# Optimization experiments

Hardware: AMD Instinct MI355X
Metric: run time of the kernel (lower is better)

The kernel has to match this reference:

```python
import jax, jax.numpy as jnp
import numpy as np

E = 1024
H = 16
DFF = 4 * E
EPS = 1e-5


def layer_norm(x, scale, bias):
    mu = jnp.mean(x, axis=-1, keepdims=True)
    var = jnp.var(x, axis=-1, keepdims=True)
    return (x - mu) * jax.lax.rsqrt(var + EPS) * scale + bias


def setup_inputs() -> dict:
    key = jax.random.key(0)
    ks = jax.random.split(key, 12)
    N, L = 2, 2048
    x = jax.random.normal(ks[0], (N, L, E), dtype=jnp.float32)
    attn_mask = jax.random.randint(ks[1], (N, H, L, L), 0, 2) == 1
    s = 0.02
    return {
        "x": x,
        "attn_mask": attn_mask,
        "ln1_s": jnp.ones((E,), jnp.float32),
        "ln1_b": jnp.zeros((E,), jnp.float32),
        "Wqkv": jax.random.normal(ks[2], (E, 3 * E), jnp.float32) * s,
        "bqkv": jnp.zeros((3 * E,), jnp.float32),
        "Wo": jax.random.normal(ks[3], (E, E), jnp.float32) * s,
        "bo": jnp.zeros((E,), jnp.float32),
        "ln2_s": jnp.ones((E,), jnp.float32),
        "ln2_b": jnp.zeros((E,), jnp.float32),
        "lnf_s": jnp.ones((E,), jnp.float32),
        "lnf_b": jnp.zeros((E,), jnp.float32),
        "W1": jax.random.normal(ks[4], (E, DFF), jnp.float32) * s,
        "b1": jnp.zeros((DFF,), jnp.float32),
        "W2": jax.random.normal(ks[5], (DFF, E), jnp.float32) * s,
        "b2": jnp.zeros((E,), jnp.float32),
    }


def reference(x, attn_mask, ln1_s, ln1_b, Wqkv, bqkv, Wo, bo,
              ln2_s, ln2_b, lnf_s, lnf_b, W1, b1, W2, b2):
    N, L, _ = x.shape
    D = E // H
    # --- self attention (pre-norm) ---
    h = layer_norm(x, ln1_s, ln1_b)
    qkv = h @ Wqkv + bqkv                      # [N,L,3E]
    q, k, v = jnp.split(qkv, 3, axis=-1)
    q = q.reshape(N, L, H, D)
    k = k.reshape(N, L, H, D)
    v = v.reshape(N, L, H, D)
    a = jnp.einsum('nqhd,nkhd->nhqk', q, k) * (D ** -0.5)  # [N,H,L,L]
    a = jnp.where(attn_mask, -jnp.inf, a)
    a = jax.nn.softmax(a, axis=-1)
    o = jnp.einsum('nhqk,nkhd->nqhd', a, v).reshape(N, L, E)
    o = o @ Wo + bo
    x = x + o
    # --- feedforward (norm_2 then FF's internal LN) ---
    h = layer_norm(x, ln2_s, ln2_b)
    h = layer_norm(h, lnf_s, lnf_b)
    h = jax.nn.gelu(h @ W1 + b1, approximate=False) @ W2 + b2
    return x + h
```

## Files before the change

kernel.cpp:

```cpp
#include <hip/hip_runtime.h>
#include <math.h>

#define E_DIM 1024
#define H_HEADS 16
#define D_HEAD 64
#define DFF_DIM 4096
#define L_SEQ 2048
#define N_BATCH 2
#define T_TOK (N_BATCH * L_SEQ)

typedef __attribute__((ext_vector_type(8))) __bf16 bf16x8;
typedef __attribute__((ext_vector_type(4))) float f32x4;

__device__ __forceinline__ unsigned short f2bf(float f) {
  union { float f; unsigned int u; } v; v.f = f;
  unsigned int r = v.u + 0x7fffu + ((v.u >> 16) & 1u);
  return (unsigned short)(r >> 16);
}

__global__ __launch_bounds__(256) void convert_transpose(
    const float* __restrict__ in, unsigned short* __restrict__ out, int K, int N) {
  __shared__ float tile[32][33];
  int n0 = blockIdx.x * 32, k0 = blockIdx.y * 32;
  int tx = threadIdx.x & 31, ty = threadIdx.x >> 5;
#pragma unroll
  for (int i = 0; i < 32; i += 8)
    tile[ty + i][tx] = in[(size_t)(k0 + ty + i) * N + n0 + tx];
  __syncthreads();
#pragma unroll
  for (int i = 0; i < 32; i += 8)
    out[(size_t)(n0 + ty + i) * K + k0 + tx] = f2bf(tile[tx][ty + i]);
}

__device__ __forceinline__ void block_reduce2(float& a, float& b, float* sm, int tid) {
#pragma unroll
  for (int off = 32; off > 0; off >>= 1) {
    a += __shfl_down(a, off);
    b += __shfl_down(b, off);
  }
  int wid = tid >> 6;
  if ((tid & 63) == 0) { sm[wid * 2] = a; sm[wid * 2 + 1] = b; }
  __syncthreads();
  a = sm[0] + sm[2] + sm[4] + sm[6];
  b = sm[1] + sm[3] + sm[5] + sm[7];
}

__global__ __launch_bounds__(256) void ln_kernel(
    const float* __restrict__ x, const float* __restrict__ s,
    const float* __restrict__ b, unsigned short* __restrict__ out) {
  int row = blockIdx.x, tid = threadIdx.x;
  __shared__ float sm[8];
  float4 v = ((const float4*)(x + (size_t)row * E_DIM))[tid];
  float sum = v.x + v.y + v.z + v.w;
  float sq = v.x * v.x + v.y * v.y + v.z * v.z + v.w * v.w;
  block_reduce2(sum, sq, sm, tid);
  float mu = sum * (1.0f / E_DIM);
  float var = sq * (1.0f / E_DIM) - mu * mu;
  float rs = rsqrtf(var + 1e-5f);
  float4 sv = ((const float4*)s)[tid];
  float4 bv = ((const float4*)b)[tid];
  ushort4 o4;
  o4.x = f2bf((v.x - mu) * rs * sv.x + bv.x);
  o4.y = f2bf((v.y - mu) * rs * sv.y + bv.y);
  o4.z = f2bf((v.z - mu) * rs * sv.z + bv.z);
  o4.w = f2bf((v.w - mu) * rs * sv.w + bv.w);
  ((ushort4*)(out + (size_t)row * E_DIM))[tid] = o4;
}

__global__ __launch_bounds__(256) void ln2_kernel(
    const float* __restrict__ x, const float* __restrict__ s2,
    const float* __restrict__ b2, const float* __restrict__ sf,
    const float* __restrict__ bf_, unsigned short* __restrict__ out) {
  int row = blockIdx.x, tid = threadIdx.x;
  __shared__ float sm[8];
  float4 v = ((const float4*)(x + (size_t)row * E_DIM))[tid];
  float sum = v.x + v.y + v.z + v.w;
  float sq = v.x * v.x + v.y * v.y + v.z * v.z + v.w * v.w;
  block_reduce2(sum, sq, sm, tid);
  float mu = sum * (1.0f / E_DIM);
  float rs = rsqrtf(sq * (1.0f / E_DIM) - mu * mu + 1e-5f);
  float4 s2v = ((const float4*)s2)[tid];
  float4 b2v = ((const float4*)b2)[tid];
  float y0 = (v.x - mu) * rs * s2v.x + b2v.x;
  float y1 = (v.y - mu) * rs * s2v.y + b2v.y;
  float y2 = (v.z - mu) * rs * s2v.z + b2v.z;
  float y3 = (v.w - mu) * rs * s2v.w + b2v.w;
  float sum2 = y0 + y1 + y2 + y3;
  float sq2 = y0 * y0 + y1 * y1 + y2 * y2 + y3 * y3;
  __syncthreads();
  block_reduce2(sum2, sq2, sm, tid);
  float mu2 = sum2 * (1.0f / E_DIM);
  float rs2 = rsqrtf(sq2 * (1.0f / E_DIM) - mu2 * mu2 + 1e-5f);
  float4 sfv = ((const float4*)sf)[tid];
  float4 bfv = ((const float4*)bf_)[tid];
  ushort4 o4;
  o4.x = f2bf((y0 - mu2) * rs2 * sfv.x + bfv.x);
  o4.y = f2bf((y1 - mu2) * rs2 * sfv.y + bfv.y);
  o4.z = f2bf((y2 - mu2) * rs2 * sfv.z + bfv.z);
  o4.w = f2bf((y3 - mu2) * rs2 * sfv.w + bfv.w);
  ((ushort4*)(out + (size_t)row * E_DIM))[tid] = o4;
}

template <int EPI>
__global__ __launch_bounds__(256) void gemm_bt(
    const unsigned short* __restrict__ A, const unsigned short* __restrict__ Bt,
    const float* __restrict__ bias, const float* __restrict__ resid,
    void* __restrict__ outp, int M, int N, int K) {
  __shared__ unsigned short As[128 * 40];
  __shared__ unsigned short Bs[128 * 40];
  int tid = threadIdx.x;
  int lane = tid & 63, wave = tid >> 6;
  int m0 = blockIdx.y * 128, n0 = blockIdx.x * 128;
  int wm = (wave & 1) * 64, wn = (wave >> 1) * 64;
  int lm = lane & 15, lq = lane >> 4;
  int trow = tid >> 2, tcol = tid & 3;
  f32x4 acc[4][4] = {};
  for (int k0 = 0; k0 < K; k0 += 32) {
    uint4 av0 = *(const uint4*)(A + (size_t)(m0 + trow) * K + k0 + tcol * 8);
    uint4 av1 = *(const uint4*)(A + (size_t)(m0 + trow + 64) * K + k0 + tcol * 8);
    uint4 bv0 = *(const uint4*)(Bt + (size_t)(n0 + trow) * K + k0 + tcol * 8);
    uint4 bv1 = *(const uint4*)(Bt + (size_t)(n0 + trow + 64) * K + k0 + tcol * 8);
    __syncthreads();
    *(uint4*)(As + trow * 40 + tcol * 8) = av0;
    *(uint4*)(As + (trow + 64) * 40 + tcol * 8) = av1;
    *(uint4*)(Bs + trow * 40 + tcol * 8) = bv0;
    *(uint4*)(Bs + (trow + 64) * 40 + tcol * 8) = bv1;
    __syncthreads();
    bf16x8 a[4], b[4];
#pragma unroll
    for (int i = 0; i < 4; i++)
      a[i] = *(const bf16x8*)(As + (wm + i * 16 + lm) * 40 + lq * 8);
#pragma unroll
    for (int j = 0; j < 4; j++)
      b[j] = *(const bf16x8*)(Bs + (wn + j * 16 + lm) * 40 + lq * 8);
#pragma unroll
    for (int i = 0; i < 4; i++)
#pragma unroll
      for (int j = 0; j < 4; j++)
        acc[i][j] = __builtin_amdgcn_mfma_f32_16x16x32_bf16(a[i], b[j], acc[i][j], 0, 0, 0);
  }
#pragma unroll
  for (int i = 0; i < 4; i++)
#pragma unroll
    for (int j = 0; j < 4; j++) {
      int row = m0 + wm + i * 16 + lq * 4;
      int col = n0 + wn + j * 16 + lm;
      float bcol = bias[col];
#pragma unroll
      for (int r = 0; r < 4; r++) {
        float v = acc[i][j][r] + bcol;
        size_t idx = (size_t)(row + r) * N + col;
        if (EPI == 0) {
          ((unsigned short*)outp)[idx] = f2bf(v);
        } else if (EPI == 1) {
          float g = 0.5f * v * (1.0f + erff(v * 0.70710678118f));
          ((unsigned short*)outp)[idx] = f2bf(g);
        } else {
          ((float*)outp)[idx] = resid[idx] + v;
        }
      }
    }
}

__global__ __launch_bounds__(256) void attn_kernel(
    const unsigned short* __restrict__ qkv, const int* __restrict__ mask,
    unsigned short* __restrict__ o) {
  const int bq = blockIdx.x;
  const int nh = blockIdx.y;
  const int h = nh & 15;
  const int tid = threadIdx.x, lane = tid & 63, wave = tid >> 6;
  const int lm = lane & 15, lq = lane >> 4;

  __shared__ unsigned short Ks[64 * 72];
  __shared__ unsigned short Vs[64 * 66];
  __shared__ unsigned short Ps[4][16 * 72];

  const int q_base = bq * 64;
  const int tok0 = (nh >> 4) * L_SEQ;
  const int qoff = h * 64, koff = E_DIM + h * 64, voff = 2 * E_DIM + h * 64;
  const int* mbase = mask + (size_t)nh * L_SEQ * L_SEQ;

  bf16x8 qf[2];
  {
    int t = tok0 + q_base + wave * 16 + lm;
    const unsigned short* qr = qkv + (size_t)t * (3 * E_DIM) + qoff + lq * 8;
    qf[0] = *(const bf16x8*)(qr);
    qf[1] = *(const bf16x8*)(qr + 32);
  }

  float m_run[4], l_run[4];
  f32x4 oacc[4] = {};
#pragma unroll
  for (int r = 0; r < 4; r++) { m_run[r] = -1e30f; l_run[r] = 0.0f; }

  for (int kt = 0; kt < L_SEQ / 64; kt++) {
    const int k_base = kt * 64;
    __syncthreads();
    {
      int row = tid >> 3, chunk = tid & 7;
#pragma unroll
      for (int it = 0; it < 2; it++) {
        int key = row + it * 32;
        int t = tok0 + k_base + key;
        uint4 kv = *(const uint4*)(qkv + (size_t)t * (3 * E_DIM) + koff + chunk * 8);
        *(uint4*)(Ks + key * 72 + chunk * 8) = kv;
        uint4 vv = *(const uint4*)(qkv + (size_t)t * (3 * E_DIM) + voff + chunk * 8);
        unsigned int* vw = (unsigned int*)(Vs + key * 66 + chunk * 8);
        vw[0] = vv.x; vw[1] = vv.y; vw[2] = vv.z; vw[3] = vv.w;
      }
    }
    __syncthreads();

    f32x4 s[4];
#pragma unroll
    for (int nt = 0; nt < 4; nt++) {
      bf16x8 kb0 = *(const bf16x8*)(Ks + (nt * 16 + lm) * 72 + lq * 8);
      bf16x8 kb1 = *(const bf16x8*)(Ks + (nt * 16 + lm) * 72 + 32 + lq * 8);
      f32x4 acc = {};
      acc = __builtin_amdgcn_mfma_f32_16x16x32_bf16(qf[0], kb0, acc, 0, 0, 0);
      acc = __builtin_amdgcn_mfma_f32_16x16x32_bf16(qf[1], kb1, acc, 0, 0, 0);
      s[nt] = acc;
    }
    const int qrow = q_base + wave * 16 + lq * 4;
#pragma unroll
    for (int nt = 0; nt < 4; nt++) {
      int kcol = k_base + nt * 16 + lm;
#pragma unroll
      for (int r = 0; r < 4; r++) {
        float v = s[nt][r] * 0.125f;
        int mval = mbase[(size_t)(qrow + r) * L_SEQ + kcol];
        s[nt][r] = mval ? -1e30f : v;
      }
    }
    float alpha[4], rsum[4];
#pragma unroll
    for (int r = 0; r < 4; r++) {
      float v = fmaxf(fmaxf(s[0][r], s[1][r]), fmaxf(s[2][r], s[3][r]));
#pragma unroll
      for (int mo = 1; mo < 16; mo <<= 1) v = fmaxf(v, __shfl_xor(v, mo));
      float mn = fmaxf(m_run[r], v);
      alpha[r] = __expf(m_run[r] - mn);
      m_run[r] = mn;
      rsum[r] = 0.0f;
    }
    unsigned short* pw = Ps[wave];
#pragma unroll
    for (int nt = 0; nt < 4; nt++)
#pragma unroll
      for (int r = 0; r < 4; r++) {
        float p = __expf(s[nt][r] - m_run[r]);
        rsum[r] += p;
        pw[(lq * 4 + r) * 72 + nt * 16 + lm] = f2bf(p);
      }
#pragma unroll
    for (int r = 0; r < 4; r++) {
      float v = rsum[r];
#pragma unroll
      for (int mo = 1; mo < 16; mo <<= 1) v += __shfl_xor(v, mo);
      l_run[r] = l_run[r] * alpha[r] + v;
    }
#pragma unroll
    for (int j = 0; j < 4; j++)
#pragma unroll
      for (int r = 0; r < 4; r++) oacc[j][r] *= alpha[r];
    __syncthreads();

#pragma unroll
    for (int c = 0; c < 2; c++) {
      bf16x8 pa = *(const bf16x8*)(pw + lm * 72 + c * 32 + lq * 8);
#pragma unroll
      for (int j = 0; j < 4; j++) {
        bf16x8 vb;
#pragma unroll
        for (int jj = 0; jj < 8; jj++)
          vb[jj] = *(const __bf16*)(Vs + (c * 32 + lq * 8 + jj) * 66 + j * 16 + lm);
        oacc[j] = __builtin_amdgcn_mfma_f32_16x16x32_bf16(pa, vb, oacc[j], 0, 0, 0);
      }
    }
  }
  const int qrow = q_base + wave * 16 + lq * 4;
#pragma unroll
  for (int r = 0; r < 4; r++) {
    float inv_l = 1.0f / l_run[r];
    int t = tok0 + qrow + r;
#pragma unroll
    for (int j = 0; j < 4; j++)
      o[(size_t)t * E_DIM + h * 64 + j * 16 + lm] = f2bf(oacc[j][r] * inv_l);
  }
}

extern "C" void kernel_launch(void* const* d_in, const int* in_sizes, int n_in,
                              void* d_out, int out_size, void* d_ws, size_t ws_size,
                              hipStream_t stream) {
  const float* x = (const float*)d_in[0];
  const int* mask = (const int*)d_in[1];
  const float* ln1_s = (const float*)d_in[2];
  const float* ln1_b = (const float*)d_in[3];
  const float* Wqkv = (const float*)d_in[4];
  const float* bqkv = (const float*)d_in[5];
  const float* Wo = (const float*)d_in[6];
  const float* bo = (const float*)d_in[7];
  const float* ln2_s = (const float*)d_in[8];
  const float* ln2_b = (const float*)d_in[9];
  const float* lnf_s = (const float*)d_in[10];
  const float* lnf_b = (const float*)d_in[11];
  const float* W1 = (const float*)d_in[12];
  const float* b1 = (const float*)d_in[13];
  const float* W2 = (const float*)d_in[14];
  const float* b2 = (const float*)d_in[15];

  size_t off = 0;
  auto alloc = [&](size_t bytes) {
    void* p = (char*)d_ws + off;
    off += (bytes + 255) & ~(size_t)255;
    return p;
  };
  unsigned short* WqkvT = (unsigned short*)alloc((size_t)3072 * 1024 * 2);
  unsigned short* WoT = (unsigned short*)alloc((size_t)1024 * 1024 * 2);
  unsigned short* W1T = (unsigned short*)alloc((size_t)4096 * 1024 * 2);
  unsigned short* W2T = (unsigned short*)alloc((size_t)1024 * 4096 * 2);
  unsigned short* h1 = (unsigned short*)alloc((size_t)T_TOK * E_DIM * 2);
  unsigned short* qkvb = (unsigned short*)alloc((size_t)T_TOK * 3 * E_DIM * 2);
  unsigned short* ob = (unsigned short*)alloc((size_t)T_TOK * E_DIM * 2);
  float* x2 = (float*)alloc((size_t)T_TOK * E_DIM * 4);
  unsigned short* h2 = (unsigned short*)alloc((size_t)T_TOK * E_DIM * 2);
  unsigned short* g1 = (unsigned short*)alloc((size_t)T_TOK * DFF_DIM * 2);

  convert_transpose<<<dim3(3072 / 32, 1024 / 32), 256, 0, stream>>>(Wqkv, WqkvT, 1024, 3072);
  convert_transpose<<<dim3(1024 / 32, 1024 / 32), 256, 0, stream>>>(Wo, WoT, 1024, 1024);
  convert_transpose<<<dim3(4096 / 32, 1024 / 32), 256, 0, stream>>>(W1, W1T, 1024, 4096);
  convert_transpose<<<dim3(1024 / 32, 4096 / 32), 256, 0, stream>>>(W2, W2T, 4096, 1024);
  ln_kernel<<<T_TOK, 256, 0, stream>>>(x, ln1_s, ln1_b, h1);
  gemm_bt<0><<<dim3(3072 / 128, T_TOK / 128), 256, 0, stream>>>(
      h1, WqkvT, bqkv, nullptr, qkvb, T_TOK, 3072, 1024);
  attn_kernel<<<dim3(L_SEQ / 64, N_BATCH * H_HEADS), 256, 0, stream>>>(qkvb, mask, ob);
  gemm_bt<2><<<dim3(1024 / 128, T_TOK / 128), 256, 0, stream>>>(
      ob, WoT, bo, x, x2, T_TOK, 1024, 1024);
  ln2_kernel<<<T_TOK, 256, 0, stream>>>(x2, ln2_s, ln2_b, lnf_s, lnf_b, h2);
  gemm_bt<1><<<dim3(DFF_DIM / 128, T_TOK / 128), 256, 0, stream>>>(
      h2, W1T, b1, nullptr, g1, T_TOK, DFF_DIM, 1024);
  gemm_bt<2><<<dim3(1024 / 128, T_TOK / 128), 256, 0, stream>>>(
      g1, W2T, b2, x2, (float*)d_out, T_TOK, 1024, 4096);

  (void)in_sizes; (void)n_in; (void)out_size; (void)ws_size;
}
```

Measured before the change: 1.073 ms.

## Use direct global-to-LDS loads, swizzled K tiles, and transposed V in attention

The GEMM tile loads now go straight from global memory into LDS with the global_load_lds builtin, which removes the register staging and the padded LDS rows. In attention, K tiles are also loaded directly into LDS with an XOR swizzle to avoid bank conflicts, and V is stored transposed so each MFMA B operand is one vector LDS read instead of eight scalar reads. Mask loads are issued early, before the tile barrier, so their latency overlaps the LDS fill. The risks are bank conflicts in the unpadded GEMM LDS layout, scattered 2-byte writes for the V transpose, and correctness of the LDS placement that global_load_lds implies.

```diff
diff --git a/kernel.cpp b/kernel.cpp
--- a/kernel.cpp
+++ b/kernel.cpp
@@ -16,6 +16,12 @@
   union { float f; unsigned int u; } v; v.f = f;
   unsigned int r = v.u + 0x7fffu + ((v.u >> 16) & 1u);
   return (unsigned short)(r >> 16);
+}
+
+__device__ __forceinline__ void gl2lds16(const void* g, void* l) {
+  __builtin_amdgcn_global_load_lds(
+      (const __attribute__((address_space(1))) unsigned int*)g,
+      (__attribute__((address_space(3))) unsigned int*)l, 16, 0, 0);
 }
 
 __global__ __launch_bounds__(256) void convert_transpose(
@@ -106,33 +112,37 @@
     const unsigned short* __restrict__ A, const unsigned short* __restrict__ Bt,
     const float* __restrict__ bias, const float* __restrict__ resid,
     void* __restrict__ outp, int M, int N, int K) {
-  __shared__ unsigned short As[128 * 40];
-  __shared__ unsigned short Bs[128 * 40];
+  __shared__ unsigned short As[128 * 32];
+  __shared__ unsigned short Bs[128 * 32];
   int tid = threadIdx.x;
   int lane = tid & 63, wave = tid >> 6;
   int m0 = blockIdx.y * 128, n0 = blockIdx.x * 128;
   int wm = (wave & 1) * 64, wn = (wave >> 1) * 64;
   int lm = lane & 15, lq = lane >> 4;
-  int trow = tid >> 2, tcol = tid & 3;
+
+  int r0 = tid >> 2, coff = (tid & 3) * 8;
+  const unsigned short* Abase = A + (size_t)m0 * K;
+  const unsigned short* Bbase = Bt + (size_t)n0 * K;
+  unsigned short* lA0 = As + (tid >> 6) * 512;
+  unsigned short* lA1 = As + 2048 + (tid >> 6) * 512;
+  unsigned short* lB0 = Bs + (tid >> 6) * 512;
+  unsigned short* lB1 = Bs + 2048 + (tid >> 6) * 512;
+
   f32x4 acc[4][4] = {};
   for (int k0 = 0; k0 < K; k0 += 32) {
-    uint4 av0 = *(const uint4*)(A + (size_t)(m0 + trow) * K + k0 + tcol * 8);
-    uint4 av1 = *(const uint4*)(A + (size_t)(m0 + trow + 64) * K + k0 + tcol * 8);
-    uint4 bv0 = *(const uint4*)(Bt + (size_t)(n0 + trow) * K + k0 + tcol * 8);
-    uint4 bv1 = *(const uint4*)(Bt + (size_t)(n0 + trow + 64) * K + k0 + tcol * 8);
-    __syncthreads();
-    *(uint4*)(As + trow * 40 + tcol * 8) = av0;
-    *(uint4*)(As + (trow + 64) * 40 + tcol * 8) = av1;
-    *(uint4*)(Bs + trow * 40 + tcol * 8) = bv0;
-    *(uint4*)(Bs + (trow + 64) * 40 + tcol * 8) = bv1;
+    __syncthreads();
+    gl2lds16(Abase + (size_t)r0 * K + k0 + coff, lA0);
+    gl2lds16(Abase + (size_t)(r0 + 64) * K + k0 + coff, lA1);
+    gl2lds16(Bbase + (size_t)r0 * K + k0 + coff, lB0);
+    gl2lds16(Bbase + (size_t)(r0 + 64) * K + k0 + coff, lB1);
     __syncthreads();
     bf16x8 a[4], b[4];
 #pragma unroll
     for (int i = 0; i < 4; i++)
-      a[i] = *(const bf16x8*)(As + (wm + i * 16 + lm) * 40 + lq * 8);
+      a[i] = *(const bf16x8*)(As + (wm + i * 16 + lm) * 32 + lq * 8);
 #pragma unroll
     for (int j = 0; j < 4; j++)
-      b[j] = *(const bf16x8*)(Bs + (wn + j * 16 + lm) * 40 + lq * 8);
+      b[j] = *(const bf16x8*)(Bs + (wn + j * 16 + lm) * 32 + lq * 8);
 #pragma unroll
     for (int i = 0; i < 4; i++)
 #pragma unroll
@@ -171,8 +181,8 @@
   const int tid = threadIdx.x, lane = tid & 63, wave = tid >> 6;
   const int lm = lane & 15, lq = lane >> 4;
 
-  __shared__ unsigned short Ks[64 * 72];
-  __shared__ unsigned short Vs[64 * 66];
+  __shared__ unsigned short Ks[64 * 64];
+  __shared__ unsigned short Vt[64 * 72];
   __shared__ unsigned short Ps[4][16 * 72];
 
   const int q_base = bq * 64;
@@ -188,6 +198,12 @@
     qf[1] = *(const bf16x8*)(qr + 32);
   }
 
+  const int sk0 = tid >> 3, sc0 = tid & 7;
+  unsigned short* lK0 = Ks + (tid >> 6) * 512;
+  unsigned short* lK1 = Ks + 2048 + (tid >> 6) * 512;
+  const int vkey = tid >> 3, vchunk = tid & 7;
+  const int qrow = q_base + wave * 16 + lq * 4;
+
   float m_run[4], l_run[4];
   f32x4 oacc[4] = {};
 #pragma unroll
@@ -196,17 +212,26 @@
   for (int kt = 0; kt < L_SEQ / 64; kt++) {
     const int k_base = kt * 64;
     __syncthreads();
+    gl2lds16(qkv + (size_t)(tok0 + k_base + sk0) * (3 * E_DIM) + koff +
+                 ((sc0 ^ (sk0 & 7)) * 8), lK0);
+    gl2lds16(qkv + (size_t)(tok0 + k_base + sk0 + 32) * (3 * E_DIM) + koff +
+                 ((sc0 ^ ((sk0 + 32) & 7)) * 8), lK1);
+    uint4 vv0 = *(const uint4*)(qkv + (size_t)(tok0 + k_base + vkey) * (3 * E_DIM) + voff + vchunk * 8);
+    uint4 vv1 = *(const uint4*)(qkv + (size_t)(tok0 + k_base + vkey + 32) * (3 * E_DIM) + voff + vchunk * 8);
+    int mv[4][4];
+#pragma unroll
+    for (int nt = 0; nt < 4; nt++)
+#pragma unroll
+      for (int r = 0; r < 4; r++)
+        mv[nt][r] = mbase[(size_t)(qrow + r) * L_SEQ + k_base + nt * 16 + lm];
     {
-      int row = tid >> 3, chunk = tid & 7;
-#pragma unroll
-      for (int it = 0; it < 2; it++) {
-        int key = row + it * 32;
-        int t = tok0 + k_base + key;
-        uint4 kv = *(const uint4*)(qkv + (size_t)t * (3 * E_DIM) + koff + chunk * 8);
-        *(uint4*)(Ks + key * 72 + chunk * 8) = kv;
-        uint4 vv = *(const uint4*)(qkv + (size_t)t * (3 * E_DIM) + voff + chunk * 8);
-        unsigned int* vw = (unsigned int*)(Vs + key * 66 + chunk * 8);
-        vw[0] = vv.x; vw[1] = vv.y; vw[2] = vv.z; vw[3] = vv.w;
+      const unsigned short* p0 = (const unsigned short*)&vv0;
+      const unsigned short* p1 = (const unsigned short*)&vv1;
+#pragma unroll
+      for (int jj = 0; jj < 8; jj++) {
+        int jx = (jj + vchunk) & 7;
+        Vt[(vchunk * 8 + jx) * 72 + vkey] = p0[jx];
+        Vt[(vchunk * 8 + jx) * 72 + vkey + 32] = p1[jx];
       }
     }
     __syncthreads();
@@ -214,24 +239,21 @@
     f32x4 s[4];
 #pragma unroll
     for (int nt = 0; nt < 4; nt++) {
-      bf16x8 kb0 = *(const bf16x8*)(Ks + (nt * 16 + lm) * 72 + lq * 8);
-      bf16x8 kb1 = *(const bf16x8*)(Ks + (nt * 16 + lm) * 72 + 32 + lq * 8);
+      int key = nt * 16 + lm, sw = key & 7;
+      bf16x8 kb0 = *(const bf16x8*)(Ks + key * 64 + ((lq ^ sw) * 8));
+      bf16x8 kb1 = *(const bf16x8*)(Ks + key * 64 + (((lq + 4) ^ sw) * 8));
       f32x4 acc = {};
       acc = __builtin_amdgcn_mfma_f32_16x16x32_bf16(qf[0], kb0, acc, 0, 0, 0);
       acc = __builtin_amdgcn_mfma_f32_16x16x32_bf16(qf[1], kb1, acc, 0, 0, 0);
       s[nt] = acc;
     }
-    const int qrow = q_base + wave * 16 + lq * 4;
-#pragma unroll
-    for (int nt = 0; nt < 4; nt++) {
-      int kcol = k_base + nt * 16 + lm;
+#pragma unroll
+    for (int nt = 0; nt < 4; nt++)
 #pragma unroll
       for (int r = 0; r < 4; r++) {
         float v = s[nt][r] * 0.125f;
-        int mval = mbase[(size_t)(qrow + r) * L_SEQ + kcol];
-        s[nt][r] = mval ? -1e30f : v;
-      }
-    }
+        s[nt][r] = mv[nt][r] ? -1e30f : v;
+      }
     float alpha[4], rsum[4];
 #pragma unroll
     for (int r = 0; r < 4; r++) {
@@ -270,15 +292,11 @@
       bf16x8 pa = *(const bf16x8*)(pw + lm * 72 + c * 32 + lq * 8);
 #pragma unroll
       for (int j = 0; j < 4; j++) {
-        bf16x8 vb;
-#pragma unroll
-        for (int jj = 0; jj < 8; jj++)
-          vb[jj] = *(const __bf16*)(Vs + (c * 32 + lq * 8 + jj) * 66 + j * 16 + lm);
+        bf16x8 vb = *(const bf16x8*)(Vt + (j * 16 + lm) * 72 + c * 32 + lq * 8);
         oacc[j] = __builtin_amdgcn_mfma_f32_16x16x32_bf16(pa, vb, oacc[j], 0, 0, 0);
       }
     }
   }
-  const int qrow = q_base + wave * 16 + lq * 4;
 #pragma unroll
   for (int r = 0; r < 4; r++) {
     float inv_l = 1.0f / l_run[r];
```

Measured after the change: 1.153 ms. +7.5%, slower.
